# Kernel tuning notes

Measured on AMD Instinct MI355X. Metric: run time of the kernel, lower is better.

Reference implementation:

```python
import jax, jax.numpy as jnp
import numpy as np


def setup_inputs() -> dict:
    key = jax.random.key(0)
    k1, k2 = jax.random.split(key)
    C, K, H, W = 512, 150, 512, 512
    feats_chw = jax.random.normal(k1, (C, H, W), dtype=jnp.float32)
    class_logits_chw = jax.random.normal(k2, (K, H, W), dtype=jnp.float32)
    return {"feats_chw": feats_chw, "class_logits_chw": class_logits_chw}


def reference(feats_chw, class_logits_chw):
    Cf, H, W = feats_chw.shape
    K = class_logits_chw.shape[0]
    N = H * W
    feats = feats_chw.reshape(Cf, N).T                      # (N, C)
    logits = class_logits_chw.reshape(K, N).T               # (N, K)
    probs = jax.nn.softmax(logits, axis=-1)                 # softmax over classes per pixel
    # normalize each class column over all N pixels
    weights = probs / jnp.clip(jnp.sum(probs, axis=0, keepdims=True), 1e-06)
    context = jnp.einsum('nk,nc->kc', weights, feats)        # (K, C)
    return context
```

## Files before the change

### kernel.cpp

```cpp
#include <hip/hip_runtime.h>
#include <hip/hip_bf16.h>


#define N_PIX (512 * 512)
#define K_CLS 150
#define C_DIM 512
#define KPAD 160

typedef short short8 __attribute__((ext_vector_type(8)));
typedef float floatx4 __attribute__((ext_vector_type(4)));

__device__ __forceinline__ unsigned short f2bf(float x) {
  unsigned u = __builtin_bit_cast(unsigned, x);
  u += 0x7FFFu + ((u >> 16) & 1u);
  return (unsigned short)(u >> 16);
}

__device__ __forceinline__ void async_ld16(const void* g, void* l) {
  __builtin_amdgcn_global_load_lds(
      (const __attribute__((address_space(1))) void*)g,
      (__attribute__((address_space(3))) void*)l, 16, 0, 0);
}
__device__ __forceinline__ void async_ld4(const void* g, void* l) {
  __builtin_amdgcn_global_load_lds(
      (const __attribute__((address_space(1))) void*)g,
      (__attribute__((address_space(3))) void*)l, 4, 0, 0);
}

#define K1_PIX 256
#define K1_NCH 8

__global__ __launch_bounds__(512, 6) void sg_softmax(
    const float* __restrict__ logits, unsigned short* __restrict__ pg,
    float* __restrict__ colsum_g)
{
  __shared__ float lraw[2][152][32];
  __shared__ float part[16][32];
  __shared__ float csum[K_CLS];

  const int tid  = threadIdx.x;
  const int w    = tid >> 6;
  const int lane = tid & 63;
  const int hi   = lane >> 5;
  const int px   = lane & 31;
  const int nbase = blockIdx.x * K1_PIX;

  if (tid < K_CLS) csum[tid] = 0.f;

  auto stage = [&](int ci, int buf) {
#pragma unroll
    for (int u = 0; u < 3; ++u) {
      const int t = w + 8 * u;
      if (t < 19) {
        int row = 8 * t + (lane >> 3);
        if (row > 149) row = 149;
        async_ld16(logits + (size_t)row * N_PIX + nbase + ci * 32 + (lane & 7) * 4,
                   &lraw[buf][8 * t][0]);
      }
    }
  };
  stage(0, 0);

  for (int ci = 0; ci < K1_NCH; ++ci) {
    const int buf = ci & 1;
    __syncthreads();

    float sp = 0.f;
    const int g = 2 * w + hi;
#pragma unroll
    for (int i = 0; i < 10; ++i) {
      const int k = g + 16 * i;
      if (k < K_CLS) sp += __expf(lraw[buf][k][px]);
    }
    part[g][px] = sp;
    __syncthreads();
    float s = 0.f;
#pragma unroll
    for (int gg = 0; gg < 16; ++gg) s += part[gg][px];
    const float rs = 1.0f / s;

    if (ci + 1 < K1_NCH) stage(ci + 1, buf ^ 1);

#pragma unroll
    for (int i = 0; i < 10; ++i) {
      const int k = w + 16 * i + 8 * hi;
      if (k < K_CLS) {
        const float p = __expf(lraw[buf][k][px]) * rs;
        pg[(size_t)k * N_PIX + nbase + ci * 32 + px] = f2bf(p);
        float r = p;
        r += __shfl_xor(r, 16);
        r += __shfl_xor(r, 8);
        r += __shfl_xor(r, 4);
        r += __shfl_xor(r, 2);
        r += __shfl_xor(r, 1);
        if (px == 0) csum[k] += r;
      }
    }
  }
  __syncthreads();
  if (tid < K_CLS) atomicAdd(&colsum_g[tid], csum[tid]);
}

#define K2_PIX 1024
#define K2_NCH 16

__global__ __launch_bounds__(512, 4) void sg_gemm(
    const float* __restrict__ feats, const unsigned short* __restrict__ pg,
    float* __restrict__ ctx)
{
  __shared__ unsigned short atile[2][20 * 64 * 8];

  const int tid  = threadIdx.x;
  const int w    = tid >> 6;
  const int lane = tid & 63;
  const int quad = lane >> 4;
  const int l15  = lane & 15;
  const int pxbase = (blockIdx.x >> 1) * K2_PIX;
  const int cbase  = (blockIdx.x & 1) * 256;

  auto stage = [&](int ci, int buf) {
#pragma unroll
    for (int u = 0; u < 3; ++u) {
      const int t = w + 8 * u;
      if (t < 20) {
        const int rg = t >> 1, ks = t & 1;
        async_ld16(pg + (size_t)(rg * 16 + l15) * N_PIX + pxbase + ci * 64 + ks * 32 + quad * 8,
                   &atile[buf][t * 512]);
      }
    }
  };

  floatx4 acc[2][10];
#pragma unroll
  for (int j = 0; j < 2; ++j)
#pragma unroll
    for (int rg = 0; rg < 10; ++rg)
      acc[j][rg] = (floatx4){0.f, 0.f, 0.f, 0.f};

  stage(0, 0);

  for (int ci = 0; ci < K2_NCH; ++ci) {
    const int buf = ci & 1;
    const int n0  = pxbase + ci * 64;
    __syncthreads();

    floatx4 breg[4];
#pragma unroll
    for (int j = 0; j < 2; ++j) {
      const float* bp = feats + (size_t)(cbase + (w + 8 * j) * 16 + l15) * N_PIX + n0 + quad * 8;
      breg[2 * j]     = *(const floatx4*)bp;
      breg[2 * j + 1] = *(const floatx4*)(bp + 4);
    }

    if (ci + 1 < K2_NCH) stage(ci + 1, buf ^ 1);

    short8 bfrag[2];
#pragma unroll
    for (int j = 0; j < 2; ++j) {
      floatx4 lo = breg[2 * j], hi = breg[2 * j + 1];
      short8 f;
      f[0] = f2bf(lo[0]); f[1] = f2bf(lo[1]); f[2] = f2bf(lo[2]); f[3] = f2bf(lo[3]);
      f[4] = f2bf(hi[0]); f[5] = f2bf(hi[1]); f[6] = f2bf(hi[2]); f[7] = f2bf(hi[3]);
      bfrag[j] = f;
    }

    floatx4 breg2[4];
#pragma unroll
    for (int j = 0; j < 2; ++j) {
      const float* bp = feats + (size_t)(cbase + (w + 8 * j) * 16 + l15) * N_PIX + n0 + 32 + quad * 8;
      breg2[2 * j]     = *(const floatx4*)bp;
      breg2[2 * j + 1] = *(const floatx4*)(bp + 4);
    }

#pragma unroll
    for (int rg = 0; rg < 10; ++rg) {
      short8 afrag = *(const short8*)&atile[buf][(rg * 2 + 0) * 512 + lane * 8];
#pragma unroll
      for (int j = 0; j < 2; ++j)
        acc[j][rg] = __builtin_amdgcn_mfma_f32_16x16x32_bf16(afrag, bfrag[j], acc[j][rg], 0, 0, 0);
    }

#pragma unroll
    for (int j = 0; j < 2; ++j) {
      floatx4 lo = breg2[2 * j], hi = breg2[2 * j + 1];
      short8 f;
      f[0] = f2bf(lo[0]); f[1] = f2bf(lo[1]); f[2] = f2bf(lo[2]); f[3] = f2bf(lo[3]);
      f[4] = f2bf(hi[0]); f[5] = f2bf(hi[1]); f[6] = f2bf(hi[2]); f[7] = f2bf(hi[3]);
      bfrag[j] = f;
    }

#pragma unroll
    for (int rg = 0; rg < 10; ++rg) {
      short8 afrag = *(const short8*)&atile[buf][(rg * 2 + 1) * 512 + lane * 8];
#pragma unroll
      for (int j = 0; j < 2; ++j)
        acc[j][rg] = __builtin_amdgcn_mfma_f32_16x16x32_bf16(afrag, bfrag[j], acc[j][rg], 0, 0, 0);
    }
  }

#pragma unroll
  for (int j = 0; j < 2; ++j) {
    const int c = cbase + ((w + 8 * j) << 4) + l15;
#pragma unroll
    for (int rg = 0; rg < 10; ++rg) {
#pragma unroll
      for (int r = 0; r < 4; ++r) {
        const int row = rg * 16 + quad * 4 + r;
        if (row < K_CLS) atomicAdd(&ctx[row * C_DIM + c], acc[j][rg][r]);
      }
    }
  }
}

__global__ void sg_epi(const float* __restrict__ ctx, const float* __restrict__ colsum,
                       float* __restrict__ out)
{
  const int idx = blockIdx.x * 256 + threadIdx.x;
  if (idx < K_CLS * C_DIM) {
    const float d = fmaxf(colsum[idx >> 9], 1e-6f);
    out[idx] = ctx[idx] / d;
  }
}

#define NBLK 256
#define PIX_PER_BLK (N_PIX / NBLK)
#define CHUNK 64
#define NCHUNK (PIX_PER_BLK / CHUNK)

__global__ __launch_bounds__(512) void sg_main(
    const float* __restrict__ feats, const float* __restrict__ logits,
    float* __restrict__ ctx, float* __restrict__ colsum_g)
{
  __shared__ float lraw[2][K_CLS][CHUNK];
  __shared__ unsigned short atile[20 * 64 * 8];
  __shared__ float part[8][64];
  __shared__ float colsum_lds[K_CLS];

  const int tid  = threadIdx.x;
  const int w    = tid >> 6;
  const int lane = tid & 63;
  const int quad = lane >> 4;
  const int l15  = lane & 15;
  const int nbase = blockIdx.x * PIX_PER_BLK;

  for (int i = tid; i < 20 * 64 * 8 / 2; i += 512) ((unsigned*)atile)[i] = 0u;
  if (tid < K_CLS) colsum_lds[tid] = 0.f;

  floatx4 acc[4][10];
#pragma unroll
  for (int j = 0; j < 4; ++j)
#pragma unroll
    for (int rg = 0; rg < 10; ++rg)
      acc[j][rg] = (floatx4){0.f, 0.f, 0.f, 0.f};

#pragma unroll
  for (int i = 0; i < 19; ++i) {
    const int k = w + 8 * i;
    if (k < K_CLS)
      async_ld4(logits + (size_t)k * N_PIX + nbase + lane, &lraw[0][k][0]);
  }

  for (int ci = 0; ci < NCHUNK; ++ci) {
    __syncthreads();
    const int buf = ci & 1;
    const int n0  = nbase + ci * CHUNK;

    floatx4 breg[8];
#pragma unroll
    for (int j = 0; j < 4; ++j) {
      const float* bp = feats + (size_t)((w + 8 * j) * 16 + l15) * N_PIX + n0 + quad * 8;
      breg[2 * j]     = *(const floatx4*)bp;
      breg[2 * j + 1] = *(const floatx4*)(bp + 4);
    }

    float s_part = 0.f;
#pragma unroll
    for (int i = 0; i < 19; ++i) {
      const int k = w + 8 * i;
      if (k < K_CLS) s_part += __expf(lraw[buf][k][lane]);
    }
    part[w][lane] = s_part;
    __syncthreads();
    float s = 0.f;
#pragma unroll
    for (int ww = 0; ww < 8; ++ww) s += part[ww][lane];
    const float rs = 1.0f / s;

#pragma unroll
    for (int i = 0; i < 19; ++i) {
      const int k = w + 8 * i;
      if (k < K_CLS) {
        const float p = __expf(lraw[buf][k][lane]) * rs;
        const int fid = ((k >> 4) << 1) + (lane >> 5);
        const int lin = (k & 15) | (((lane >> 3) & 3) << 4);
        atile[(fid * 64 + lin) * 8 + (lane & 7)] = f2bf(p);
        float r = p;
        r += __shfl_xor(r, 32);
        r += __shfl_xor(r, 16);
        r += __shfl_xor(r, 8);
        r += __shfl_xor(r, 4);
        r += __shfl_xor(r, 2);
        r += __shfl_xor(r, 1);
        if (lane == 0) colsum_lds[k] += r;
      }
    }
    __syncthreads();

    short8 bfrag[4];
#pragma unroll
    for (int j = 0; j < 4; ++j) {
      floatx4 lo = breg[2 * j], hi = breg[2 * j + 1];
      short8 f;
      f[0] = f2bf(lo[0]); f[1] = f2bf(lo[1]); f[2] = f2bf(lo[2]); f[3] = f2bf(lo[3]);
      f[4] = f2bf(hi[0]); f[5] = f2bf(hi[1]); f[6] = f2bf(hi[2]); f[7] = f2bf(hi[3]);
      bfrag[j] = f;
    }

#pragma unroll
    for (int j = 0; j < 4; ++j) {
      const float* bp = feats + (size_t)((w + 8 * j) * 16 + l15) * N_PIX + n0 + 32 + quad * 8;
      breg[2 * j]     = *(const floatx4*)bp;
      breg[2 * j + 1] = *(const floatx4*)(bp + 4);
    }

    if (ci + 1 < NCHUNK) {
#pragma unroll
      for (int i = 0; i < 19; ++i) {
        const int k = w + 8 * i;
        if (k < K_CLS)
          async_ld4(logits + (size_t)k * N_PIX + n0 + CHUNK + lane, &lraw[buf ^ 1][k][0]);
      }
    }

#pragma unroll
    for (int rg = 0; rg < 10; ++rg) {
      short8 afrag = *(const short8*)&atile[((rg * 2 + 0) * 64 + lane) * 8];
#pragma unroll
      for (int j = 0; j < 4; ++j)
        acc[j][rg] = __builtin_amdgcn_mfma_f32_16x16x32_bf16(afrag, bfrag[j], acc[j][rg], 0, 0, 0);
    }

#pragma unroll
    for (int j = 0; j < 4; ++j) {
      floatx4 lo = breg[2 * j], hi = breg[2 * j + 1];
      short8 f;
      f[0] = f2bf(lo[0]); f[1] = f2bf(lo[1]); f[2] = f2bf(lo[2]); f[3] = f2bf(lo[3]);
      f[4] = f2bf(hi[0]); f[5] = f2bf(hi[1]); f[6] = f2bf(hi[2]); f[7] = f2bf(hi[3]);
      bfrag[j] = f;
    }

#pragma unroll
    for (int rg = 0; rg < 10; ++rg) {
      short8 afrag = *(const short8*)&atile[((rg * 2 + 1) * 64 + lane) * 8];
#pragma unroll
      for (int j = 0; j < 4; ++j)
        acc[j][rg] = __builtin_amdgcn_mfma_f32_16x16x32_bf16(afrag, bfrag[j], acc[j][rg], 0, 0, 0);
    }
  }

#pragma unroll
  for (int j = 0; j < 4; ++j) {
    const int c = ((w + 8 * j) << 4) + l15;
#pragma unroll
    for (int rg = 0; rg < 10; ++rg) {
#pragma unroll
      for (int r = 0; r < 4; ++r) {
        const int row = rg * 16 + quad * 4 + r;
        if (row < K_CLS) atomicAdd(&ctx[row * C_DIM + c], acc[j][rg][r]);
      }
    }
  }
  __syncthreads();
  if (tid < K_CLS) atomicAdd(&colsum_g[tid], colsum_lds[tid]);
}

extern "C" void kernel_launch(void* const* d_in, const int* in_sizes, int n_in,
                              void* d_out, int out_size, void* d_ws, size_t ws_size,
                              hipStream_t stream)
{
  const float* feats  = (const float*)d_in[0];
  const float* logits = (const float*)d_in[1];

  const size_t pg_bytes = (size_t)KPAD * N_PIX * sizeof(unsigned short);
  const size_t acc_bytes = (size_t)(K_CLS * C_DIM + K_CLS) * sizeof(float);

  if (ws_size >= pg_bytes + acc_bytes) {
    unsigned short* pg = (unsigned short*)d_ws;
    float* ctx    = (float*)((char*)d_ws + pg_bytes);
    float* colsum = ctx + K_CLS * C_DIM;
    hipMemsetAsync(ctx, 0, acc_bytes, stream);
    sg_softmax<<<dim3(1024), dim3(512), 0, stream>>>(logits, pg, colsum);
    sg_gemm<<<dim3(512), dim3(512), 0, stream>>>(feats, pg, ctx);
    sg_epi<<<dim3((K_CLS * C_DIM + 255) / 256), dim3(256), 0, stream>>>(ctx, colsum, (float*)d_out);
  } else {
    float* ctx    = (float*)d_ws;
    float* colsum = ctx + K_CLS * C_DIM;
    hipMemsetAsync(d_ws, 0, acc_bytes, stream);
    sg_main<<<dim3(NBLK), dim3(512), 0, stream>>>(feats, logits, ctx, colsum);
    sg_epi<<<dim3((K_CLS * C_DIM + 255) / 256), dim3(256), 0, stream>>>(ctx, colsum, (float*)d_out);
  }
}
```

Baseline: 930.1 us.

## Replace GEMM atomics with per-partition slabs and a deterministic reduction epilogue

The GEMM kernel now writes each pixel-partition's partial K×C context tile into its own slab in workspace with plain stores, instead of issuing float atomicAdds into one shared accumulator. A new epilogue kernel sums the 256 partitions and applies the column-sum normalisation. The block-to-work mapping is also remapped to spread partitions across blocks. This removes atomic contention but adds about 80MB of slab writes and reads, and the workspace size check is larger, so a small workspace falls back to the other path.

```diff
diff --git a/kernel.cpp b/kernel.cpp
--- a/kernel.cpp
+++ b/kernel.cpp
@@ -6,6 +6,7 @@
 #define K_CLS 150
 #define C_DIM 512
 #define KPAD 160
+#define NPART 256
 
 typedef short short8 __attribute__((ext_vector_type(8)));
 typedef float floatx4 __attribute__((ext_vector_type(4)));
@@ -106,7 +107,7 @@
 
 __global__ __launch_bounds__(512, 4) void sg_gemm(
     const float* __restrict__ feats, const unsigned short* __restrict__ pg,
-    float* __restrict__ ctx)
+    float* __restrict__ slab)
 {
   __shared__ unsigned short atile[2][20 * 64 * 8];
 
@@ -115,8 +116,13 @@
   const int lane = tid & 63;
   const int quad = lane >> 4;
   const int l15  = lane & 15;
-  const int pxbase = (blockIdx.x >> 1) * K2_PIX;
-  const int cbase  = (blockIdx.x & 1) * 256;
+
+  const int x      = blockIdx.x & 7;
+  const int g      = blockIdx.x >> 3;
+  const int chalf  = g & 1;
+  const int pxpart = (g >> 1) | (x << 5);
+  const int pxbase = pxpart * K2_PIX;
+  const int cbase  = chalf * 256;
 
   auto stage = [&](int ci, int buf) {
 #pragma unroll
@@ -198,18 +204,37 @@
     }
   }
 
+  float* sb = slab + (size_t)pxpart * (KPAD * C_DIM) + cbase;
 #pragma unroll
   for (int j = 0; j < 2; ++j) {
-    const int c = cbase + ((w + 8 * j) << 4) + l15;
+    const int c = ((w + 8 * j) << 4) + l15;
 #pragma unroll
     for (int rg = 0; rg < 10; ++rg) {
 #pragma unroll
       for (int r = 0; r < 4; ++r) {
         const int row = rg * 16 + quad * 4 + r;
-        if (row < K_CLS) atomicAdd(&ctx[row * C_DIM + c], acc[j][rg][r]);
-      }
-    }
-  }
+        sb[row * C_DIM + c] = acc[j][rg][r];
+      }
+    }
+  }
+}
+
+__global__ void sg_epi2(const float* __restrict__ slab, const float* __restrict__ colsum,
+                        float* __restrict__ out)
+{
+  const int idx = blockIdx.x * 256 + threadIdx.x;
+  if (idx >= K_CLS * C_DIM) return;
+  const size_t stride = (size_t)KPAD * C_DIM;
+  float s0 = 0.f, s1 = 0.f, s2 = 0.f, s3 = 0.f;
+#pragma unroll 4
+  for (int p = 0; p < NPART; p += 4) {
+    s0 += slab[(size_t)(p + 0) * stride + idx];
+    s1 += slab[(size_t)(p + 1) * stride + idx];
+    s2 += slab[(size_t)(p + 2) * stride + idx];
+    s3 += slab[(size_t)(p + 3) * stride + idx];
+  }
+  const float d = fmaxf(colsum[idx >> 9], 1e-6f);
+  out[idx] = ((s0 + s1) + (s2 + s3)) / d;
 }
 
 __global__ void sg_epi(const float* __restrict__ ctx, const float* __restrict__ colsum,
@@ -381,21 +406,22 @@
   const float* feats  = (const float*)d_in[0];
   const float* logits = (const float*)d_in[1];
 
-  const size_t pg_bytes = (size_t)KPAD * N_PIX * sizeof(unsigned short);
-  const size_t acc_bytes = (size_t)(K_CLS * C_DIM + K_CLS) * sizeof(float);
-
-  if (ws_size >= pg_bytes + acc_bytes) {
+  const size_t pg_bytes   = (size_t)KPAD * N_PIX * sizeof(unsigned short);
+  const size_t slab_bytes = (size_t)NPART * KPAD * C_DIM * sizeof(float);
+  const size_t colsum_bytes = (size_t)K_CLS * sizeof(float);
+
+  if (ws_size >= pg_bytes + slab_bytes + colsum_bytes) {
     unsigned short* pg = (unsigned short*)d_ws;
-    float* ctx    = (float*)((char*)d_ws + pg_bytes);
-    float* colsum = ctx + K_CLS * C_DIM;
-    hipMemsetAsync(ctx, 0, acc_bytes, stream);
+    float* slab   = (float*)((char*)d_ws + pg_bytes);
+    float* colsum = (float*)((char*)d_ws + pg_bytes + slab_bytes);
+    hipMemsetAsync(colsum, 0, colsum_bytes, stream);
     sg_softmax<<<dim3(1024), dim3(512), 0, stream>>>(logits, pg, colsum);
-    sg_gemm<<<dim3(512), dim3(512), 0, stream>>>(feats, pg, ctx);
-    sg_epi<<<dim3((K_CLS * C_DIM + 255) / 256), dim3(256), 0, stream>>>(ctx, colsum, (float*)d_out);
+    sg_gemm<<<dim3(512), dim3(512), 0, stream>>>(feats, pg, slab);
+    sg_epi2<<<dim3((K_CLS * C_DIM + 255) / 256), dim3(256), 0, stream>>>(slab, colsum, (float*)d_out);
   } else {
     float* ctx    = (float*)d_ws;
     float* colsum = ctx + K_CLS * C_DIM;
-    hipMemsetAsync(d_ws, 0, acc_bytes, stream);
+    hipMemsetAsync(d_ws, 0, (K_CLS * C_DIM + K_CLS) * sizeof(float), stream);
     sg_main<<<dim3(NBLK), dim3(512), 0, stream>>>(feats, logits, ctx, colsum);
     sg_epi<<<dim3((K_CLS * C_DIM + 255) / 256), dim3(256), 0, stream>>>(ctx, colsum, (float*)d_out);
   }
```

New measurement: 937.4 us. No clear change (+0.8%).
